# Performance work log

Measured on AMD Instinct MI355X. Metric: run time of the kernel, lower is better.

Reference implementation:

```python
import jax, jax.numpy as jnp
from jax import lax
import numpy as np

MARGIN = 0.3
N, D = 4096, 2048          # batch, global feat dim
C, PARTS = 128, 8          # local feature channels, horizontal stripes
K_PER_ID = 4               # instances per identity (equal counts required by hard mining)
EPS = 1e-12


def batch_euclidean_dist(x, y):
    # x: [N, m, d], y: [N, n, d] -> [N, m, n]
    xx = jnp.sum(x * x, axis=-1)[:, :, None]
    yy = jnp.sum(y * y, axis=-1)[:, None, :]
    d2 = xx + yy - 2.0 * jnp.einsum('bmd,bnd->bmn', x, y)
    return jnp.sqrt(jnp.clip(d2, EPS))


def shortest_dist(dist_mat):
    # dist_mat: [m, n, N] -> [N]; DTW-style monotone shortest path DP.
    # dist[i][j] = min(dist[i-1][j], dist[i][j-1]) + dist_mat[i, j]
    row0 = jnp.cumsum(dist_mat[0], axis=0)  # [n, N]

    def row_step(prev_row, dm_i):  # prev_row: [n, N], dm_i: [n, N]
        first = prev_row[0] + dm_i[0]

        def col_step(left, args):
            prev_j, dm_ij = args
            cur = jnp.minimum(prev_j, left) + dm_ij
            return cur, cur

        _, rest = lax.scan(col_step, first, (prev_row[1:], dm_i[1:]))
        row = jnp.concatenate([first[None], rest], axis=0)
        return row, None

    last_row, _ = lax.scan(row_step, row0, dist_mat[1:])
    return last_row[-1]


def batch_local_dist(x, y):
    # x: [N, m, d], y: [N, n, d] -> [N]
    dm = batch_euclidean_dist(x, y)
    # (exp(d)-1)/(exp(d)+1) == tanh(d/2)
    dm = jnp.tanh(dm * 0.5)
    return shortest_dist(jnp.transpose(dm, (1, 2, 0)))


def setup_inputs() -> dict:
    key = jax.random.key(0)
    k1, k2 = jax.random.split(key)
    inputs = jax.random.normal(k1, (N, D), dtype=jnp.float32)
    local_features = jax.random.normal(k2, (N, C, PARTS), dtype=jnp.float32)
    targets = jnp.arange(N, dtype=jnp.int32) // K_PER_ID  # equal #samples per id
    return {"inputs": inputs, "targets": targets, "local_features": local_features}


def reference(inputs, targets, local_features):
    # L2 normalize global features
    norm = jnp.linalg.norm(inputs, axis=-1, keepdims=True)
    feats = inputs / (norm + EPS)

    # pairwise euclidean distance [N, N]
    sq = jnp.sum(feats * feats, axis=1)
    d2 = sq[:, None] + sq[None, :] - 2.0 * (feats @ feats.T)
    dist = jnp.sqrt(jnp.clip(d2, EPS))

    # hard example mining (self counts as positive, as in torch mask)
    is_pos = targets[:, None] == targets[None, :]
    pos_d = jnp.where(is_pos, dist, -jnp.inf)
    neg_d = jnp.where(is_pos, jnp.inf, dist)
    dist_ap = jnp.max(pos_d, axis=1)
    dist_an = jnp.min(neg_d, axis=1)
    p_inds = jnp.argmax(pos_d, axis=1)
    n_inds = jnp.argmin(neg_d, axis=1)

    # local branch: [N, C, parts] -> [N, parts, C]
    lf = jnp.transpose(local_features, (0, 2, 1))
    local_dist_ap = batch_local_dist(lf, lf[p_inds])
    local_dist_an = batch_local_dist(lf, lf[n_inds])

    # MarginRankingLoss with y=1, mean reduction: mean(relu(margin - (an - ap)))
    global_loss = jnp.mean(jax.nn.relu(MARGIN - (dist_an - dist_ap)))
    local_loss = jnp.mean(jax.nn.relu(MARGIN - (local_dist_an - local_dist_ap)))
    return (global_loss, local_loss)
```

## Files before the change

kernel.cpp:

```cpp
#include <hip/hip_runtime.h>
#include <hip/hip_bf16.h>
#include <math.h>

#define NB    4096
#define DD    2048
#define CLOC  128
#define PARTS 8
#define FEPS  1e-12f
#define FMARGIN 0.3f
#define NCHUNK 16

typedef short bf16x8 __attribute__((ext_vector_type(8)));
typedef float f32x4 __attribute__((ext_vector_type(4)));

#define GLD16(g, l) __builtin_amdgcn_global_load_lds(                          \
    (const __attribute__((address_space(1))) void*)(g),                        \
    (__attribute__((address_space(3))) void*)(l), 16, 0, 0)

__global__ __launch_bounds__(256) void normalize_pack_kernel(
    const float* __restrict__ x, uint4* __restrict__ Hp, uint4* __restrict__ Lp,
    float* __restrict__ sq) {
  __shared__ float sm[4];
  const int t = threadIdx.x;
  const int lane = t & 63, wid = t >> 6;
  const int r0 = blockIdx.x * 4;
  uint4 hreg[4], lreg[4];
#pragma unroll
  for (int q = 0; q < 4; ++q) {
    const int row = r0 + q;
    const float* xr = x + (size_t)row * DD + 8 * t;
    const float4 a = *(const float4*)xr;
    const float4 b = *(const float4*)(xr + 4);
    float v[8] = {a.x, a.y, a.z, a.w, b.x, b.y, b.z, b.w};
    float ss = 0.f;
#pragma unroll
    for (int j = 0; j < 8; ++j) ss += v[j] * v[j];
    for (int off = 32; off; off >>= 1) ss += __shfl_down(ss, off);
    if (lane == 0) sm[wid] = ss;
    __syncthreads();
    const float tot = sm[0] + sm[1] + sm[2] + sm[3];
    __syncthreads();
    const float inv = 1.0f / (sqrtf(tot) + FEPS);
    if (t == 0) sq[row] = tot * inv * inv;
    unsigned int hw[4], lw[4];
#pragma unroll
    for (int jp = 0; jp < 4; ++jp) {
      const float f0 = v[2 * jp] * inv, f1 = v[2 * jp + 1] * inv;
      const __hip_bfloat16 h0 = __float2bfloat16(f0), h1 = __float2bfloat16(f1);
      const float l0 = f0 - __bfloat162float(h0);
      const float l1 = f1 - __bfloat162float(h1);
      const __hip_bfloat16 g0 = __float2bfloat16(l0), g1 = __float2bfloat16(l1);
      hw[jp] = (unsigned)__builtin_bit_cast(unsigned short, h0) |
               ((unsigned)__builtin_bit_cast(unsigned short, h1) << 16);
      lw[jp] = (unsigned)__builtin_bit_cast(unsigned short, g0) |
               ((unsigned)__builtin_bit_cast(unsigned short, g1) << 16);
    }
    hreg[q] = make_uint4(hw[0], hw[1], hw[2], hw[3]);
    lreg[q] = make_uint4(lw[0], lw[1], lw[2], lw[3]);
  }
  uint4* hd = Hp + (size_t)t * NB + r0;
  uint4* ld = Lp + (size_t)t * NB + r0;
#pragma unroll
  for (int q = 0; q < 4; ++q) { hd[q] = hreg[q]; ld[q] = lreg[q]; }
}

#define BMT 128
#define KSTEP 32
#define NKT (DD / KSTEP)
#define CHUNK_COLS 256

__global__ __launch_bounds__(256, 2) void dist_mine_mfma(
    const uint4* __restrict__ Hp, const uint4* __restrict__ Lp,
    const float* __restrict__ sq, const int* __restrict__ targets,
    float* __restrict__ pap, int* __restrict__ papi,
    float* __restrict__ pan, int* __restrict__ pani) {
  __shared__ __attribute__((aligned(16))) char lds[2][32768];
  __shared__ float redv[2][2][BMT];
  __shared__ int   redi[2][2][BMT];
  const int tid = threadIdx.x;
  const int lane = tid & 63;
  const int w = tid >> 6;
  const int wr = w >> 1, wc = w & 1;
  const int g = lane >> 4, cl = lane & 15;
  const int rowtile = blockIdx.x >> 4;
  const int chunk = blockIdx.x & 15;
  const int row0 = rowtile * BMT;
  const int chunk0 = chunk * CHUNK_COLS;

  float bap[16], ban[16];
  int bapi[16], bani[16];
#pragma unroll
  for (int k = 0; k < 16; ++k) {
    bap[k] = -INFINITY; ban[k] = INFINITY; bapi[k] = 0; bani[k] = 0;
  }

  auto stage = [&](int p) {
    const int ct = p >> 6, kt = p & (NKT - 1);
    const int col0 = chunk0 + ct * BMT;
    const int r = tid & 127;
    const int shalf = tid >> 7;
    char* lbase = lds[p & 1];
#pragma unroll
    for (int u = 0; u < 8; ++u) {
      const int q = u >> 1;
      const int s = (u & 1) * 2 + shalf;
      const int baserow = (q & 2) ? col0 : row0;
      const uint4* src = (q & 1) ? Lp : Hp;
      const uint4* gp = src + (size_t)(kt * 4 + s) * NB + baserow + r;
      GLD16(gp, lbase + u * 4096 + tid * 16);
    }
  };

  stage(0);
  __syncthreads();

  f32x4 acc[4][4];
#pragma unroll
  for (int m = 0; m < 4; ++m)
#pragma unroll
    for (int n = 0; n < 4; ++n) acc[m][n] = (f32x4){0.f, 0.f, 0.f, 0.f};

  for (int p = 0; p < 2 * NKT; ++p) {
    if (p + 1 < 2 * NKT) stage(p + 1);
    const char* base = lds[p & 1];
    const int aoff = g * 2048 + (wr * 64 + cl) * 16;
    const int boff = g * 2048 + (wc * 64 + cl) * 16;
    bf16x8 aH[4], bH[4], aL[4], bL[4];
#pragma unroll
    for (int m = 0; m < 4; ++m) aH[m] = *(const bf16x8*)(base + aoff + m * 256);
#pragma unroll
    for (int n = 0; n < 4; ++n) bH[n] = *(const bf16x8*)(base + 16384 + boff + n * 256);
#pragma unroll
    for (int m = 0; m < 4; ++m)
#pragma unroll
      for (int n = 0; n < 4; ++n)
        acc[m][n] = __builtin_amdgcn_mfma_f32_16x16x32_bf16(aH[m], bH[n], acc[m][n], 0, 0, 0);
#pragma unroll
    for (int m = 0; m < 4; ++m) aL[m] = *(const bf16x8*)(base + 8192 + aoff + m * 256);
#pragma unroll
    for (int m = 0; m < 4; ++m)
#pragma unroll
      for (int n = 0; n < 4; ++n)
        acc[m][n] = __builtin_amdgcn_mfma_f32_16x16x32_bf16(aL[m], bH[n], acc[m][n], 0, 0, 0);
#pragma unroll
    for (int n = 0; n < 4; ++n) bL[n] = *(const bf16x8*)(base + 24576 + boff + n * 256);
#pragma unroll
    for (int m = 0; m < 4; ++m)
#pragma unroll
      for (int n = 0; n < 4; ++n)
        acc[m][n] = __builtin_amdgcn_mfma_f32_16x16x32_bf16(aH[m], bL[n], acc[m][n], 0, 0, 0);
    __syncthreads();

    if ((p & (NKT - 1)) == NKT - 1) {
      const int ct = p >> 6;
      const int colb = chunk0 + ct * BMT + wc * 64;
#pragma unroll
      for (int n = 0; n < 4; ++n) {
        const int col = colb + n * 16 + cl;
        const float sqc = sq[col];
        const int tgc = targets[col];
#pragma unroll
        for (int m = 0; m < 4; ++m)
#pragma unroll
          for (int i = 0; i < 4; ++i) {
            const int rrow = row0 + wr * 64 + m * 16 + g * 4 + i;
            const float d2 = sq[rrow] + sqc - 2.0f * acc[m][n][i];
            const float dist = sqrtf(fmaxf(d2, FEPS));
            const int k16 = m * 4 + i;
            if (tgc == targets[rrow]) {
              if (dist > bap[k16]) { bap[k16] = dist; bapi[k16] = col; }
            } else {
              if (dist < ban[k16]) { ban[k16] = dist; bani[k16] = col; }
            }
          }
      }
      if (ct == 0) {
#pragma unroll
        for (int m = 0; m < 4; ++m)
#pragma unroll
          for (int n = 0; n < 4; ++n) acc[m][n] = (f32x4){0.f, 0.f, 0.f, 0.f};
      }
    }
  }

#pragma unroll
  for (int off = 1; off < 16; off <<= 1) {
#pragma unroll
    for (int k = 0; k < 16; ++k) {
      const float v = __shfl_xor(bap[k], off); const int vi = __shfl_xor(bapi[k], off);
      if (v > bap[k] || (v == bap[k] && vi < bapi[k])) { bap[k] = v; bapi[k] = vi; }
      const float u2 = __shfl_xor(ban[k], off); const int ui = __shfl_xor(bani[k], off);
      if (u2 < ban[k] || (u2 == ban[k] && ui < bani[k])) { ban[k] = u2; bani[k] = ui; }
    }
  }
  if (cl == 0) {
#pragma unroll
    for (int m = 0; m < 4; ++m)
#pragma unroll
      for (int i = 0; i < 4; ++i) {
        const int rl = wr * 64 + m * 16 + g * 4 + i;
        redv[0][wc][rl] = bap[m * 4 + i]; redi[0][wc][rl] = bapi[m * 4 + i];
        redv[1][wc][rl] = ban[m * 4 + i]; redi[1][wc][rl] = bani[m * 4 + i];
      }
  }
  __syncthreads();
  if (tid < BMT) {
    const int row = row0 + tid;
    float pv = redv[0][0][tid]; int pi = redi[0][0][tid];
    const float v1 = redv[0][1][tid]; const int i1 = redi[0][1][tid];
    if (v1 > pv || (v1 == pv && i1 < pi)) { pv = v1; pi = i1; }
    float nv = redv[1][0][tid]; int ni = redi[1][0][tid];
    const float v2 = redv[1][1][tid]; const int i2 = redi[1][1][tid];
    if (v2 < nv || (v2 == nv && i2 < ni)) { nv = v2; ni = i2; }
    pap[row * NCHUNK + chunk] = pv; papi[row * NCHUNK + chunk] = pi;
    pan[row * NCHUNK + chunk] = nv; pani[row * NCHUNK + chunk] = ni;
  }
}

__global__ __launch_bounds__(256) void mine_reduce_kernel(
    const float* __restrict__ pap, const int* __restrict__ papi,
    const float* __restrict__ pan, const int* __restrict__ pani,
    float* __restrict__ dap, float* __restrict__ dan,
    int* __restrict__ pidx, int* __restrict__ nidx) {
  const int row = blockIdx.x * 256 + threadIdx.x;
  if (row >= NB) return;
  float bap = -INFINITY, ban = INFINITY;
  int bapi = 0, bani = 0;
#pragma unroll
  for (int c = 0; c < NCHUNK; ++c) {
    const float v = pap[row * NCHUNK + c]; const int i2 = papi[row * NCHUNK + c];
    if (v > bap || (v == bap && i2 < bapi)) { bap = v; bapi = i2; }
    const float w = pan[row * NCHUNK + c]; const int j2 = pani[row * NCHUNK + c];
    if (w < ban || (w == ban && j2 < bani)) { ban = w; bani = j2; }
  }
  dap[row] = bap; dan[row] = ban; pidx[row] = bapi; nidx[row] = bani;
}

__global__ __launch_bounds__(64) void local_dist_kernel(
    const float* __restrict__ lf,
    const int* __restrict__ pidx, const int* __restrict__ nidx,
    float* __restrict__ lap, float* __restrict__ lan) {
  const int i = blockIdx.x;
  const int j = (blockIdx.y == 0) ? pidx[i] : nidx[i];
  __shared__ float X[CLOC * PARTS];
  __shared__ float Y[CLOC * PARTS];
  __shared__ float DM[64];
  const int t = threadIdx.x;
  const float* xi = lf + (size_t)i * (CLOC * PARTS);
  const float* yj = lf + (size_t)j * (CLOC * PARTS);
  for (int e = t; e < CLOC * PARTS; e += 64) { X[e] = xi[e]; Y[e] = yj[e]; }
  __syncthreads();
  const int p = t >> 3, q = t & 7;
  float xx = 0.f, yy = 0.f, xy = 0.f;
#pragma unroll 8
  for (int c = 0; c < CLOC; ++c) {
    const float xv = X[c * 8 + p], yv = Y[c * 8 + q];
    xx += xv * xv; yy += yv * yv; xy += xv * yv;
  }
  const float d2 = xx + yy - 2.0f * xy;
  const float dist = sqrtf(fmaxf(d2, FEPS));
  DM[p * 8 + q] = tanhf(0.5f * dist);
  __syncthreads();
  if (t == 0) {
    float row[8];
    row[0] = DM[0];
    for (int c = 1; c < 8; ++c) row[c] = row[c - 1] + DM[c];
    for (int r = 1; r < 8; ++r) {
      row[0] += DM[r * 8];
      for (int c = 1; c < 8; ++c) row[c] = fminf(row[c], row[c - 1]) + DM[r * 8 + c];
    }
    ((blockIdx.y == 0) ? lap : lan)[i] = row[7];
  }
}

__global__ __launch_bounds__(256) void loss_kernel(
    const float* __restrict__ dap, const float* __restrict__ dan,
    const float* __restrict__ lap, const float* __restrict__ lan,
    float* __restrict__ out) {
  __shared__ float sm1[4], sm2[4];
  const int t = threadIdx.x;
  float s1 = 0.f, s2 = 0.f;
  for (int i = t; i < NB; i += 256) {
    s1 += fmaxf(0.f, FMARGIN - (dan[i] - dap[i]));
    s2 += fmaxf(0.f, FMARGIN - (lan[i] - lap[i]));
  }
  for (int off = 32; off; off >>= 1) { s1 += __shfl_down(s1, off); s2 += __shfl_down(s2, off); }
  const int lane = t & 63, wid = t >> 6;
  if (lane == 0) { sm1[wid] = s1; sm2[wid] = s2; }
  __syncthreads();
  if (t == 0) {
    out[0] = (sm1[0] + sm1[1] + sm1[2] + sm1[3]) * (1.0f / NB);
    out[1] = (sm2[0] + sm2[1] + sm2[2] + sm2[3]) * (1.0f / NB);
  }
}

extern "C" void kernel_launch(void* const* d_in, const int* in_sizes, int n_in,
                              void* d_out, int out_size, void* d_ws, size_t ws_size,
                              hipStream_t stream) {
  const float* inputs = (const float*)d_in[0];
  const int* targets = (const int*)d_in[1];
  const float* localf = (const float*)d_in[2];
  float* out = (float*)d_out;

  uint4* Hp  = (uint4*)d_ws;
  uint4* Lp  = Hp + (size_t)(DD / 8) * NB;
  float* sq  = (float*)(Lp + (size_t)(DD / 8) * NB);
  float* pap = sq + NB;
  int*   papi = (int*)(pap + (size_t)NB * NCHUNK);
  float* pan  = (float*)(papi + (size_t)NB * NCHUNK);
  int*   pani = (int*)(pan + (size_t)NB * NCHUNK);
  float* dap  = (float*)(pani + (size_t)NB * NCHUNK);
  float* dan  = dap + NB;
  int*   pidx = (int*)(dan + NB);
  int*   nidx = pidx + NB;
  float* lap  = (float*)(nidx + NB);
  float* lan  = lap + NB;

  normalize_pack_kernel<<<NB / 4, 256, 0, stream>>>(inputs, Hp, Lp, sq);
  dist_mine_mfma<<<(NB / BMT) * NCHUNK, 256, 0, stream>>>(Hp, Lp, sq, targets,
                                                          pap, papi, pan, pani);
  mine_reduce_kernel<<<NB / 256, 256, 0, stream>>>(pap, papi, pan, pani, dap, dan, pidx, nidx);
  local_dist_kernel<<<dim3(NB, 2), 64, 0, stream>>>(localf, pidx, nidx, lap, lan);
  loss_kernel<<<1, 256, 0, stream>>>(dap, dan, lap, lan, out);
}
```

Measured before the change: 319.6 us.

## Exploit distance-matrix symmetry: compute upper-triangular tiles, mine rows and columns

The distance GEMM now launches one block per 128x128 tile on or below the diagonal, not over the full N×N matrix. Each block mines hard positives and negatives along both its rows and its columns, writing partial results for both tile indices. The aim is to roughly halve the MFMA work of the dominant kernel, at the cost of an extra column-direction reduction and more shared memory per block. Separately, the local-distance kernel is merged so one 128-thread block handles both the positive and negative pair and loads the anchor features once.

```diff
diff --git a/kernel.cpp b/kernel.cpp
--- a/kernel.cpp
+++ b/kernel.cpp
@@ -8,7 +8,7 @@
 #define PARTS 8
 #define FEPS  1e-12f
 #define FMARGIN 0.3f
-#define NCHUNK 16
+#define NCHUNK 32
 
 typedef short bf16x8 __attribute__((ext_vector_type(8)));
 typedef float f32x4 __attribute__((ext_vector_type(4)));
@@ -67,7 +67,7 @@
 #define BMT 128
 #define KSTEP 32
 #define NKT (DD / KSTEP)
-#define CHUNK_COLS 256
+#define NTILES ((NB / BMT) * (NB / BMT + 1) / 2)
 
 __global__ __launch_bounds__(256, 2) void dist_mine_mfma(
     const uint4* __restrict__ Hp, const uint4* __restrict__ Lp,
@@ -75,31 +75,28 @@
     float* __restrict__ pap, int* __restrict__ papi,
     float* __restrict__ pan, int* __restrict__ pani) {
   __shared__ __attribute__((aligned(16))) char lds[2][32768];
-  __shared__ float redv[2][2][BMT];
-  __shared__ int   redi[2][2][BMT];
+  __shared__ float rowv[2][2][BMT];
+  __shared__ int   rowi[2][2][BMT];
+  __shared__ float colv[2][2][BMT];
+  __shared__ int   coli[2][2][BMT];
   const int tid = threadIdx.x;
   const int lane = tid & 63;
   const int w = tid >> 6;
   const int wr = w >> 1, wc = w & 1;
   const int g = lane >> 4, cl = lane & 15;
-  const int rowtile = blockIdx.x >> 4;
-  const int chunk = blockIdx.x & 15;
-  const int row0 = rowtile * BMT;
-  const int chunk0 = chunk * CHUNK_COLS;
-
-  float bap[16], ban[16];
-  int bapi[16], bani[16];
-#pragma unroll
-  for (int k = 0; k < 16; ++k) {
-    bap[k] = -INFINITY; ban[k] = INFINITY; bapi[k] = 0; bani[k] = 0;
-  }
-
-  auto stage = [&](int p) {
-    const int ct = p >> 6, kt = p & (NKT - 1);
-    const int col0 = chunk0 + ct * BMT;
+
+  const int tb = blockIdx.x;
+  int I = (int)((sqrtf(8.0f * tb + 1.0f) - 1.0f) * 0.5f);
+  while ((I + 1) * (I + 2) / 2 <= tb) ++I;
+  while (I * (I + 1) / 2 > tb) --I;
+  const int J = tb - I * (I + 1) / 2;
+  const int row0 = I * BMT;
+  const int col0 = J * BMT;
+
+  auto stage = [&](int kt) {
     const int r = tid & 127;
     const int shalf = tid >> 7;
-    char* lbase = lds[p & 1];
+    char* lbase = lds[kt & 1];
 #pragma unroll
     for (int u = 0; u < 8; ++u) {
       const int q = u >> 1;
@@ -120,8 +117,8 @@
 #pragma unroll
     for (int n = 0; n < 4; ++n) acc[m][n] = (f32x4){0.f, 0.f, 0.f, 0.f};
 
-  for (int p = 0; p < 2 * NKT; ++p) {
-    if (p + 1 < 2 * NKT) stage(p + 1);
+  for (int p = 0; p < NKT; ++p) {
+    if (p + 1 < NKT) stage(p + 1);
     const char* base = lds[p & 1];
     const int aoff = g * 2048 + (wr * 64 + cl) * 16;
     const int boff = g * 2048 + (wc * 64 + cl) * 16;
@@ -150,70 +147,135 @@
       for (int n = 0; n < 4; ++n)
         acc[m][n] = __builtin_amdgcn_mfma_f32_16x16x32_bf16(aH[m], bL[n], acc[m][n], 0, 0, 0);
     __syncthreads();
-
-    if ((p & (NKT - 1)) == NKT - 1) {
-      const int ct = p >> 6;
-      const int colb = chunk0 + ct * BMT + wc * 64;
+  }
+
+  float rsq[4][4]; int rtg[4][4];
+#pragma unroll
+  for (int m = 0; m < 4; ++m)
+#pragma unroll
+    for (int i = 0; i < 4; ++i) {
+      const int rr = row0 + wr * 64 + m * 16 + g * 4 + i;
+      rsq[m][i] = sq[rr]; rtg[m][i] = targets[rr];
+    }
+  float csq[4]; int ctg[4];
+#pragma unroll
+  for (int n = 0; n < 4; ++n) {
+    const int cc = col0 + wc * 64 + n * 16 + cl;
+    csq[n] = sq[cc]; ctg[n] = targets[cc];
+  }
+#pragma unroll
+  for (int m = 0; m < 4; ++m)
+#pragma unroll
+    for (int n = 0; n < 4; ++n)
+#pragma unroll
+      for (int i = 0; i < 4; ++i)
+        acc[m][n][i] = sqrtf(fmaxf(rsq[m][i] + csq[n] - 2.0f * acc[m][n][i], FEPS));
+
+  {
+    float bap[16], ban[16]; int bapi[16], bani[16];
+#pragma unroll
+    for (int k = 0; k < 16; ++k) {
+      bap[k] = -INFINITY; ban[k] = INFINITY; bapi[k] = 0; bani[k] = 0;
+    }
+#pragma unroll
+    for (int n = 0; n < 4; ++n) {
+      const int col = col0 + wc * 64 + n * 16 + cl;
+#pragma unroll
+      for (int m = 0; m < 4; ++m)
+#pragma unroll
+        for (int i = 0; i < 4; ++i) {
+          const float d = acc[m][n][i];
+          const int k16 = m * 4 + i;
+          if (ctg[n] == rtg[m][i]) {
+            if (d > bap[k16] || (d == bap[k16] && col < bapi[k16])) { bap[k16] = d; bapi[k16] = col; }
+          } else {
+            if (d < ban[k16] || (d == ban[k16] && col < bani[k16])) { ban[k16] = d; bani[k16] = col; }
+          }
+        }
+    }
+#pragma unroll
+    for (int off = 1; off < 16; off <<= 1) {
+#pragma unroll
+      for (int k = 0; k < 16; ++k) {
+        const float v = __shfl_xor(bap[k], off); const int vi = __shfl_xor(bapi[k], off);
+        if (v > bap[k] || (v == bap[k] && vi < bapi[k])) { bap[k] = v; bapi[k] = vi; }
+        const float u2 = __shfl_xor(ban[k], off); const int ui = __shfl_xor(bani[k], off);
+        if (u2 < ban[k] || (u2 == ban[k] && ui < bani[k])) { ban[k] = u2; bani[k] = ui; }
+      }
+    }
+    if (cl == 0) {
+#pragma unroll
+      for (int m = 0; m < 4; ++m)
+#pragma unroll
+        for (int i = 0; i < 4; ++i) {
+          const int rl = wr * 64 + m * 16 + g * 4 + i;
+          rowv[0][wc][rl] = bap[m * 4 + i]; rowi[0][wc][rl] = bapi[m * 4 + i];
+          rowv[1][wc][rl] = ban[m * 4 + i]; rowi[1][wc][rl] = bani[m * 4 + i];
+        }
+    }
+  }
+
+  {
+    float cap[4], can[4]; int capi[4], cani[4];
+#pragma unroll
+    for (int n = 0; n < 4; ++n) { cap[n] = -INFINITY; can[n] = INFINITY; capi[n] = 0; cani[n] = 0; }
+#pragma unroll
+    for (int n = 0; n < 4; ++n) {
+#pragma unroll
+      for (int m = 0; m < 4; ++m)
+#pragma unroll
+        for (int i = 0; i < 4; ++i) {
+          const int rr = row0 + wr * 64 + m * 16 + g * 4 + i;
+          const float d = acc[m][n][i];
+          if (rtg[m][i] == ctg[n]) {
+            if (d > cap[n] || (d == cap[n] && rr < capi[n])) { cap[n] = d; capi[n] = rr; }
+          } else {
+            if (d < can[n] || (d == can[n] && rr < cani[n])) { can[n] = d; cani[n] = rr; }
+          }
+        }
+    }
+#pragma unroll
+    for (int off = 16; off < 64; off <<= 1) {
 #pragma unroll
       for (int n = 0; n < 4; ++n) {
-        const int col = colb + n * 16 + cl;
-        const float sqc = sq[col];
-        const int tgc = targets[col];
-#pragma unroll
-        for (int m = 0; m < 4; ++m)
-#pragma unroll
-          for (int i = 0; i < 4; ++i) {
-            const int rrow = row0 + wr * 64 + m * 16 + g * 4 + i;
-            const float d2 = sq[rrow] + sqc - 2.0f * acc[m][n][i];
-            const float dist = sqrtf(fmaxf(d2, FEPS));
-            const int k16 = m * 4 + i;
-            if (tgc == targets[rrow]) {
-              if (dist > bap[k16]) { bap[k16] = dist; bapi[k16] = col; }
-            } else {
-              if (dist < ban[k16]) { ban[k16] = dist; bani[k16] = col; }
-            }
-          }
+        const float v = __shfl_xor(cap[n], off); const int vi = __shfl_xor(capi[n], off);
+        if (v > cap[n] || (v == cap[n] && vi < capi[n])) { cap[n] = v; capi[n] = vi; }
+        const float u2 = __shfl_xor(can[n], off); const int ui = __shfl_xor(cani[n], off);
+        if (u2 < can[n] || (u2 == can[n] && ui < cani[n])) { can[n] = u2; cani[n] = ui; }
       }
-      if (ct == 0) {
-#pragma unroll
-        for (int m = 0; m < 4; ++m)
-#pragma unroll
-          for (int n = 0; n < 4; ++n) acc[m][n] = (f32x4){0.f, 0.f, 0.f, 0.f};
+    }
+    if (g == 0) {
+#pragma unroll
+      for (int n = 0; n < 4; ++n) {
+        const int c = wc * 64 + n * 16 + cl;
+        colv[0][wr][c] = cap[n]; coli[0][wr][c] = capi[n];
+        colv[1][wr][c] = can[n]; coli[1][wr][c] = cani[n];
       }
     }
   }
 
-#pragma unroll
-  for (int off = 1; off < 16; off <<= 1) {
-#pragma unroll
-    for (int k = 0; k < 16; ++k) {
-      const float v = __shfl_xor(bap[k], off); const int vi = __shfl_xor(bapi[k], off);
-      if (v > bap[k] || (v == bap[k] && vi < bapi[k])) { bap[k] = v; bapi[k] = vi; }
-      const float u2 = __shfl_xor(ban[k], off); const int ui = __shfl_xor(bani[k], off);
-      if (u2 < ban[k] || (u2 == ban[k] && ui < bani[k])) { ban[k] = u2; bani[k] = ui; }
-    }
-  }
-  if (cl == 0) {
-#pragma unroll
-    for (int m = 0; m < 4; ++m)
-#pragma unroll
-      for (int i = 0; i < 4; ++i) {
-        const int rl = wr * 64 + m * 16 + g * 4 + i;
-        redv[0][wc][rl] = bap[m * 4 + i]; redi[0][wc][rl] = bapi[m * 4 + i];
-        redv[1][wc][rl] = ban[m * 4 + i]; redi[1][wc][rl] = bani[m * 4 + i];
-      }
-  }
   __syncthreads();
   if (tid < BMT) {
     const int row = row0 + tid;
-    float pv = redv[0][0][tid]; int pi = redi[0][0][tid];
-    const float v1 = redv[0][1][tid]; const int i1 = redi[0][1][tid];
+    float pv = rowv[0][0][tid]; int pi = rowi[0][0][tid];
+    const float v1 = rowv[0][1][tid]; const int i1 = rowi[0][1][tid];
     if (v1 > pv || (v1 == pv && i1 < pi)) { pv = v1; pi = i1; }
-    float nv = redv[1][0][tid]; int ni = redi[1][0][tid];
-    const float v2 = redv[1][1][tid]; const int i2 = redi[1][1][tid];
+    float nv = rowv[1][0][tid]; int ni = rowi[1][0][tid];
+    const float v2 = rowv[1][1][tid]; const int i2 = rowi[1][1][tid];
     if (v2 < nv || (v2 == nv && i2 < ni)) { nv = v2; ni = i2; }
-    pap[row * NCHUNK + chunk] = pv; papi[row * NCHUNK + chunk] = pi;
-    pan[row * NCHUNK + chunk] = nv; pani[row * NCHUNK + chunk] = ni;
+    pap[row * NCHUNK + J] = pv; papi[row * NCHUNK + J] = pi;
+    pan[row * NCHUNK + J] = nv; pani[row * NCHUNK + J] = ni;
+  } else if (I != J) {
+    const int c = tid - BMT;
+    const int row = col0 + c;
+    float pv = colv[0][0][c]; int pi = coli[0][0][c];
+    const float v1 = colv[0][1][c]; const int i1 = coli[0][1][c];
+    if (v1 > pv || (v1 == pv && i1 < pi)) { pv = v1; pi = i1; }
+    float nv = colv[1][0][c]; int ni = coli[1][0][c];
+    const float v2 = colv[1][1][c]; const int i2 = coli[1][1][c];
+    if (v2 < nv || (v2 == nv && i2 < ni)) { nv = v2; ni = i2; }
+    pap[row * NCHUNK + I] = pv; papi[row * NCHUNK + I] = pi;
+    pan[row * NCHUNK + I] = nv; pani[row * NCHUNK + I] = ni;
   }
 }
 
@@ -236,40 +298,43 @@
   dap[row] = bap; dan[row] = ban; pidx[row] = bapi; nidx[row] = bani;
 }
 
-__global__ __launch_bounds__(64) void local_dist_kernel(
+__global__ __launch_bounds__(128) void local_dist_kernel(
     const float* __restrict__ lf,
     const int* __restrict__ pidx, const int* __restrict__ nidx,
     float* __restrict__ lap, float* __restrict__ lan) {
   const int i = blockIdx.x;
-  const int j = (blockIdx.y == 0) ? pidx[i] : nidx[i];
   __shared__ float X[CLOC * PARTS];
-  __shared__ float Y[CLOC * PARTS];
-  __shared__ float DM[64];
+  __shared__ float Y[2][CLOC * PARTS];
+  __shared__ float DM[2][64];
   const int t = threadIdx.x;
+  const int h = t >> 6, tl = t & 63;
+  const int j = (h == 0) ? pidx[i] : nidx[i];
   const float* xi = lf + (size_t)i * (CLOC * PARTS);
   const float* yj = lf + (size_t)j * (CLOC * PARTS);
-  for (int e = t; e < CLOC * PARTS; e += 64) { X[e] = xi[e]; Y[e] = yj[e]; }
-  __syncthreads();
-  const int p = t >> 3, q = t & 7;
+  for (int e = t; e < CLOC * PARTS; e += 128) X[e] = xi[e];
+  for (int e = tl; e < CLOC * PARTS; e += 64) Y[h][e] = yj[e];
+  __syncthreads();
+  const int p = tl >> 3, q = tl & 7;
   float xx = 0.f, yy = 0.f, xy = 0.f;
 #pragma unroll 8
   for (int c = 0; c < CLOC; ++c) {
-    const float xv = X[c * 8 + p], yv = Y[c * 8 + q];
+    const float xv = X[c * 8 + p], yv = Y[h][c * 8 + q];
     xx += xv * xv; yy += yv * yv; xy += xv * yv;
   }
   const float d2 = xx + yy - 2.0f * xy;
   const float dist = sqrtf(fmaxf(d2, FEPS));
-  DM[p * 8 + q] = tanhf(0.5f * dist);
-  __syncthreads();
-  if (t == 0) {
+  DM[h][p * 8 + q] = tanhf(0.5f * dist);
+  __syncthreads();
+  if (tl == 0) {
+    const float* dm = DM[h];
     float row[8];
-    row[0] = DM[0];
-    for (int c = 1; c < 8; ++c) row[c] = row[c - 1] + DM[c];
+    row[0] = dm[0];
+    for (int c = 1; c < 8; ++c) row[c] = row[c - 1] + dm[c];
     for (int r = 1; r < 8; ++r) {
-      row[0] += DM[r * 8];
-      for (int c = 1; c < 8; ++c) row[c] = fminf(row[c], row[c - 1]) + DM[r * 8 + c];
-    }
-    ((blockIdx.y == 0) ? lap : lan)[i] = row[7];
+      row[0] += dm[r * 8];
+      for (int c = 1; c < 8; ++c) row[c] = fminf(row[c], row[c - 1]) + dm[r * 8 + c];
+    }
+    ((h == 0) ? lap : lan)[i] = row[7];
   }
 }
 
@@ -317,9 +382,9 @@
   float* lan  = lap + NB;
 
   normalize_pack_kernel<<<NB / 4, 256, 0, stream>>>(inputs, Hp, Lp, sq);
-  dist_mine_mfma<<<(NB / BMT) * NCHUNK, 256, 0, stream>>>(Hp, Lp, sq, targets,
-                                                          pap, papi, pan, pani);
+  dist_mine_mfma<<<NTILES, 256, 0, stream>>>(Hp, Lp, sq, targets,
+                                             pap, papi, pan, pani);
   mine_reduce_kernel<<<NB / 256, 256, 0, stream>>>(pap, papi, pan, pani, dap, dan, pidx, nidx);
-  local_dist_kernel<<<dim3(NB, 2), 64, 0, stream>>>(localf, pidx, nidx, lap, lan);
+  local_dist_kernel<<<NB, 128, 0, stream>>>(localf, pidx, nidx, lap, lan);
   loss_kernel<<<1, 256, 0, stream>>>(dap, dan, lap, lan, out);
 }
```

New measurement: 320.8 us. Within noise of the previous version (+0.4%).
